# Kernel tuning notes

Hardware: AMD Instinct MI355X
Metric: run time of the kernel (lower is better)

Reference implementation:

```python
import jax, jax.numpy as jnp
import numpy as np

N_NODES = 50000
N_EDGES = 800000
IN_DIM = 128
HEADS = 8
HEAD_DIM = 16


def setup_inputs() -> dict:
    key = jax.random.key(0)
    ks = jax.random.split(key, 9)
    s = 1.0 / np.sqrt(IN_DIM)
    return {
        "h": jax.random.normal(ks[0], (N_NODES, IN_DIM), dtype=jnp.float32),
        "src": jax.random.randint(ks[1], (N_EDGES,), 0, N_NODES, dtype=jnp.int32),
        "dst": jax.random.randint(ks[2], (N_EDGES,), 0, N_NODES, dtype=jnp.int32),
        "WQ": jax.random.normal(ks[3], (IN_DIM, HEADS * HEAD_DIM), dtype=jnp.float32) * s,
        "bQ": jnp.zeros((HEADS * HEAD_DIM,), dtype=jnp.float32),
        "WK": jax.random.normal(ks[4], (IN_DIM, HEADS * HEAD_DIM), dtype=jnp.float32) * s,
        "bK": jnp.zeros((HEADS * HEAD_DIM,), dtype=jnp.float32),
        "WV": jax.random.normal(ks[5], (IN_DIM, HEADS * HEAD_DIM), dtype=jnp.float32) * s,
        "bV": jnp.zeros((HEADS * HEAD_DIM,), dtype=jnp.float32),
    }


def reference(h, src, dst, WQ, bQ, WK, bK, WV, bV):
    N = h.shape[0]
    sqrt_d = jnp.float32(np.sqrt(HEAD_DIM))
    # node projections, viewed as [N, H, D]
    Q = (h @ WQ + bQ).reshape(N, HEADS, HEAD_DIM)
    K = (h @ WK + bK).reshape(N, HEADS, HEAD_DIM)
    V = (h @ WV + bV).reshape(N, HEADS, HEAD_DIM)
    # edge scores: (K_src . Q_dst) per head, scaled exp with clamp [-5, 5]
    score = jnp.sum(K[src] * Q[dst], axis=-1, keepdims=True)  # [E, H, 1]
    score = jnp.exp(jnp.clip(score / sqrt_d, -5.0, 5.0))
    # segment-softmax denominator z and weighted V sum wV, both scattered to dst
    z = jax.ops.segment_sum(score, dst, num_segments=N)            # [N, H, 1]
    wV = jax.ops.segment_sum(V[src] * score, dst, num_segments=N)  # [N, H, D]
    # possible_empty: divide only where z > 0 (wV is 0 there anyway)
    head_out = jnp.where(z > 0, wV / jnp.where(z > 0, z, 1.0), wV)
    return head_out
```

## Files before the change

kernel.cpp:

```cpp
#include <hip/hip_runtime.h>
#include <math.h>

#define DIM 128
#define N_HEADS 8
#define HD 16
#define CAP 96

typedef __attribute__((ext_vector_type(8))) short bf16x8;
typedef __attribute__((ext_vector_type(4))) float f32x4;

__device__ __forceinline__ unsigned bf16pack2(float a, float b) {
    unsigned ua = __builtin_bit_cast(unsigned, a);
    unsigned ub = __builtin_bit_cast(unsigned, b);
    ua = (ua + 0x7FFFu + ((ua >> 16) & 1u)) >> 16;
    ub = (ub + 0x7FFFu + ((ub >> 16) & 1u)) >> 16;
    return ua | (ub << 16);
}
__device__ __forceinline__ float bf16lo(unsigned p) {
    return __builtin_bit_cast(float, p << 16);
}
__device__ __forceinline__ float bf16hi(unsigned p) {
    return __builtin_bit_cast(float, p & 0xFFFF0000u);
}

__global__ __launch_bounds__(256)
void init_kernel(const float* __restrict__ WQ, const float* __restrict__ bQ,
                 const float* __restrict__ WK, const float* __restrict__ bK,
                 const float* __restrict__ WV, const float* __restrict__ bV,
                 unsigned short* __restrict__ WT, float* __restrict__ bias384,
                 int* __restrict__ cnt, int NB, int N)
{
    if ((int)blockIdx.x < NB) {
        int i = blockIdx.x * 256 + threadIdx.x;
        if (i < N) cnt[i] = 0;
    } else {
        int idx = ((int)blockIdx.x - NB) * 256 + threadIdx.x;
        int c = idx >> 7, k = idx & 127;
        const float* W; const float* b; int col = c & 127;
        if (c < 128)      { W = WQ; b = bQ; }
        else if (c < 256) { W = WK; b = bK; }
        else              { W = WV; b = bV; }
        float v = W[k * DIM + col];
        WT[(size_t)c * DIM + k] = (unsigned short)(bf16pack2(v, 0.0f) & 0xFFFFu);
        if (k == 0) bias384[c] = b[col];
    }
}

__global__ __launch_bounds__(256)
void append_kernel(const int* __restrict__ src, const int* __restrict__ dst,
                   int* __restrict__ cnt, int* __restrict__ srcsF, int E)
{
    int e = blockIdx.x * 256 + threadIdx.x;
    if (e < E) {
        int d    = dst[e];
        int slot = atomicAdd(&cnt[d], 1);
        if (slot < CAP) srcsF[(size_t)d * CAP + slot] = src[e];
    }
}

__global__ __launch_bounds__(256)
void qkv_mfma_kernel(const float* __restrict__ h,
                     const unsigned short* __restrict__ WT,
                     const float* __restrict__ bias384,
                     unsigned* __restrict__ Qd, unsigned* __restrict__ KVd,
                     int N)
{
    __shared__ unsigned short hs[64 * 136];
    const int tid = threadIdx.x;
    const int n0  = blockIdx.x * 64;

    #pragma unroll
    for (int i = 0; i < 4; ++i) {
        int lin  = i * 256 + tid;
        int node = lin >> 4;
        int k0   = (lin & 15) * 8;
        int gn   = n0 + node;
        float4 a0, a1;
        if (gn < N) {
            a0 = *(const float4*)(h + (size_t)gn * DIM + k0);
            a1 = *(const float4*)(h + (size_t)gn * DIM + k0 + 4);
        } else {
            a0 = make_float4(0.f, 0.f, 0.f, 0.f);
            a1 = a0;
        }
        uint4 p = make_uint4(bf16pack2(a0.x, a0.y), bf16pack2(a0.z, a0.w),
                             bf16pack2(a1.x, a1.y), bf16pack2(a1.z, a1.w));
        *(uint4*)(hs + node * 136 + k0) = p;
    }
    __syncthreads();

    const int wave   = tid >> 6;
    const int l      = tid & 63;
    const int lane16 = l & 15;
    const int quad   = l >> 4;
    const int wc0    = wave * 96;

    f32x4 acc[6][4];
    #pragma unroll
    for (int ct = 0; ct < 6; ++ct) {
        float4 bv = *(const float4*)(bias384 + wc0 + ct * 16 + quad * 4);
        #pragma unroll
        for (int rt = 0; rt < 4; ++rt)
            acc[ct][rt] = (f32x4){bv.x, bv.y, bv.z, bv.w};
    }

    #pragma unroll
    for (int ks = 0; ks < 4; ++ks) {
        bf16x8 a[6], b[4];
        #pragma unroll
        for (int ct = 0; ct < 6; ++ct)
            a[ct] = *(const bf16x8*)(WT + (size_t)(wc0 + ct * 16 + lane16) * DIM
                                         + ks * 32 + quad * 8);
        #pragma unroll
        for (int rt = 0; rt < 4; ++rt)
            b[rt] = *(const bf16x8*)(hs + (rt * 16 + lane16) * 136 + ks * 32 + quad * 8);
        #pragma unroll
        for (int ct = 0; ct < 6; ++ct)
            #pragma unroll
            for (int rt = 0; rt < 4; ++rt)
                acc[ct][rt] = __builtin_amdgcn_mfma_f32_16x16x32_bf16(
                    a[ct], b[rt], acc[ct][rt], 0, 0, 0);
    }

    #pragma unroll
    for (int ct = 0; ct < 6; ++ct) {
        const int col = wc0 + ct * 16 + quad * 4;
        #pragma unroll
        for (int rt = 0; rt < 4; ++rt) {
            int gn = n0 + rt * 16 + lane16;
            if (gn >= N) continue;
            f32x4 v = acc[ct][rt];
            uint2 pr = make_uint2(bf16pack2(v[0], v[1]), bf16pack2(v[2], v[3]));
            if (col < 128) {
                *(uint2*)(Qd + (size_t)gn * 64 + (col >> 1)) = pr;
            } else if (col < 256) {
                int c = col - 128;
                *(uint2*)(KVd + (size_t)gn * 128 + ((c >> 3) * 8) + ((c & 4) >> 1)) = pr;
            } else {
                int c = col - 256;
                *(uint2*)(KVd + (size_t)gn * 128 + ((c >> 3) * 8) + 4 + ((c & 4) >> 1)) = pr;
            }
        }
    }
}

__global__ __launch_bounds__(256)
void aggregate_kernel(const int* __restrict__ cnt, const int* __restrict__ srcsF,
                      const unsigned* __restrict__ Qd, const unsigned* __restrict__ KVd,
                      float* __restrict__ out, int N)
{
    const int node = blockIdx.x * 4 + (threadIdx.x >> 6);
    if (node >= N) return;
    const int l    = threadIdx.x & 63;
    const int slot = l >> 4;
    const int c    = l & 15;

    const uint4 qd = *(const uint4*)(Qd + (size_t)node * 64 + c * 4);
    const float q0 = bf16lo(qd.x), q1 = bf16hi(qd.x);
    const float q2 = bf16lo(qd.y), q3 = bf16hi(qd.y);
    const float q4 = bf16lo(qd.z), q5 = bf16hi(qd.z);
    const float q6 = bf16lo(qd.w), q7 = bf16hi(qd.w);

    int deg = cnt[node];
    if (deg > CAP) deg = CAP;
    const int* bucket = srcsF + (size_t)node * CAP;

    float acc[8] = {0.f, 0.f, 0.f, 0.f, 0.f, 0.f, 0.f, 0.f};
    float zs = 0.f;

    for (int eg = 0; eg < deg; eg += 16) {
        bool val[4];
        const uint4* p[4];
        #pragma unroll
        for (int j = 0; j < 4; ++j) {
            int ee = eg + j * 4 + slot;
            val[j] = ee < deg;
            int s  = bucket[val[j] ? ee : (deg - 1)];
            p[j]   = (const uint4*)(KVd + (size_t)s * 128 + c * 8);
        }
        uint4 K[4], V[4];
        #pragma unroll
        for (int j = 0; j < 4; ++j) { K[j] = p[j][0]; V[j] = p[j][1]; }

        float d[4];
        #pragma unroll
        for (int j = 0; j < 4; ++j)
            d[j] = bf16lo(K[j].x) * q0 + bf16hi(K[j].x) * q1
                 + bf16lo(K[j].y) * q2 + bf16hi(K[j].y) * q3
                 + bf16lo(K[j].z) * q4 + bf16hi(K[j].z) * q5
                 + bf16lo(K[j].w) * q6 + bf16hi(K[j].w) * q7;
        #pragma unroll
        for (int j = 0; j < 4; ++j) d[j] += __shfl_xor(d[j], 1);

        #pragma unroll
        for (int j = 0; j < 4; ++j) {
            float pc = fminf(fmaxf(d[j] * 0.25f, -5.0f), 5.0f);
            float w  = val[j] ? __expf(pc) : 0.0f;
            zs += w;
            acc[0] += w * bf16lo(V[j].x); acc[1] += w * bf16hi(V[j].x);
            acc[2] += w * bf16lo(V[j].y); acc[3] += w * bf16hi(V[j].y);
            acc[4] += w * bf16lo(V[j].z); acc[5] += w * bf16hi(V[j].z);
            acc[6] += w * bf16lo(V[j].w); acc[7] += w * bf16hi(V[j].w);
        }
    }

    #pragma unroll
    for (int j = 0; j < 8; ++j) {
        acc[j] += __shfl_xor(acc[j], 16);
        acc[j] += __shfl_xor(acc[j], 32);
    }
    zs += __shfl_xor(zs, 16);
    zs += __shfl_xor(zs, 32);

    if (slot == 0) {
        float inv = (zs > 0.0f) ? (1.0f / zs) : 0.0f;
        *(float4*)(out + (size_t)node * DIM + c * 8) =
            make_float4(acc[0] * inv, acc[1] * inv, acc[2] * inv, acc[3] * inv);
        *(float4*)(out + (size_t)node * DIM + c * 8 + 4) =
            make_float4(acc[4] * inv, acc[5] * inv, acc[6] * inv, acc[7] * inv);
    }
}

extern "C" void kernel_launch(void* const* d_in, const int* in_sizes, int n_in,
                              void* d_out, int out_size, void* d_ws, size_t ws_size,
                              hipStream_t stream) {
    const float* h   = (const float*)d_in[0];
    const int*   src = (const int*)  d_in[1];
    const int*   dst = (const int*)  d_in[2];
    const float* WQ  = (const float*)d_in[3];
    const float* bQ  = (const float*)d_in[4];
    const float* WK  = (const float*)d_in[5];
    const float* bK  = (const float*)d_in[6];
    const float* WV  = (const float*)d_in[7];
    const float* bV  = (const float*)d_in[8];
    float* out = (float*)d_out;

    const int N  = in_sizes[0] / DIM;
    const int E  = in_sizes[1];
    const int NB = (N + 255) / 256;
    const int EB = (E + 255) / 256;
    const int nConv = (384 * DIM) / 256;

    char* w = (char*)d_ws;
    unsigned*       Qd      = (unsigned*)w;        w += (size_t)N * 64  * sizeof(unsigned);
    unsigned*       KVd     = (unsigned*)w;        w += (size_t)N * 128 * sizeof(unsigned);
    unsigned short* WT      = (unsigned short*)w;  w += (size_t)384 * DIM * sizeof(unsigned short);
    float*          bias384 = (float*)w;           w += 384 * sizeof(float);
    int*            cnt     = (int*)w;             w += (size_t)N * sizeof(int);
    int*            srcsF   = (int*)w;

    init_kernel<<<NB + nConv, 256, 0, stream>>>(WQ, bQ, WK, bK, WV, bV,
                                                WT, bias384, cnt, NB, N);
    append_kernel<<<EB, 256, 0, stream>>>(src, dst, cnt, srcsF, E);
    qkv_mfma_kernel<<<(N + 63) / 64, 256, 0, stream>>>(h, WT, bias384, Qd, KVd, N);
    aggregate_kernel<<<(N + 3) / 4, 256, 0, stream>>>(cnt, srcsF, Qd, KVd, out, N);
}
```

Before: 228.0 us.

## Merge edge bucketing with QKV projection and pipeline persistent aggregation

The edge-append work and the QKV MFMA projection now run in one launch, with the blocks split by index, so the scatter atomics overlap the GEMM and one launch is saved. The aggregate kernel becomes persistent: a fixed grid of 2048 blocks grid-strides over nodes and prefetches the next node's degree, Q and first 32 source indices while it processes the current one. The first two 16-edge chunks use these preloaded indices. This hides the dependent latency of loading an index and then gathering K/V, at the cost of more registers. The append blocks also allocate the 17KB shared array, which may lower their occupancy.

```diff
diff --git a/kernel.cpp b/kernel.cpp
--- a/kernel.cpp
+++ b/kernel.cpp
@@ -47,25 +47,26 @@
 }
 
 __global__ __launch_bounds__(256)
-void append_kernel(const int* __restrict__ src, const int* __restrict__ dst,
-                   int* __restrict__ cnt, int* __restrict__ srcsF, int E)
-{
-    int e = blockIdx.x * 256 + threadIdx.x;
-    if (e < E) {
-        int d    = dst[e];
-        int slot = atomicAdd(&cnt[d], 1);
-        if (slot < CAP) srcsF[(size_t)d * CAP + slot] = src[e];
-    }
-}
-
-__global__ __launch_bounds__(256)
-void qkv_mfma_kernel(const float* __restrict__ h,
-                     const unsigned short* __restrict__ WT,
-                     const float* __restrict__ bias384,
-                     unsigned* __restrict__ Qd, unsigned* __restrict__ KVd,
-                     int N)
+void append_qkv_kernel(const int* __restrict__ src, const int* __restrict__ dst,
+                       int* __restrict__ cnt, int* __restrict__ srcsF, int E, int QB,
+                       const float* __restrict__ h,
+                       const unsigned short* __restrict__ WT,
+                       const float* __restrict__ bias384,
+                       unsigned* __restrict__ Qd, unsigned* __restrict__ KVd,
+                       int N)
 {
     __shared__ unsigned short hs[64 * 136];
+
+    if ((int)blockIdx.x >= QB) {
+        int e = ((int)blockIdx.x - QB) * 256 + threadIdx.x;
+        if (e < E) {
+            int d    = dst[e];
+            int slot = atomicAdd(&cnt[d], 1);
+            if (slot < CAP) srcsF[(size_t)d * CAP + slot] = src[e];
+        }
+        return;
+    }
+
     const int tid = threadIdx.x;
     const int n0  = blockIdx.x * 64;
 
@@ -144,80 +145,134 @@
     }
 }
 
-__global__ __launch_bounds__(256)
+__device__ __forceinline__ void agg_chunk16(
+    const unsigned* __restrict__ KVd, int eg, int deg, int slot, int c,
+    const int* raw,
+    float q0, float q1, float q2, float q3,
+    float q4, float q5, float q6, float q7,
+    float acc[8], float& zs)
+{
+    bool val[4];
+    const uint4* p[4];
+    #pragma unroll
+    for (int j = 0; j < 4; ++j) {
+        int ee = eg + j * 4 + slot;
+        val[j] = ee < deg;
+        int s  = val[j] ? raw[j] : 0;
+        p[j]   = (const uint4*)(KVd + (size_t)s * 128 + c * 8);
+    }
+    uint4 K[4], V[4];
+    #pragma unroll
+    for (int j = 0; j < 4; ++j) { K[j] = p[j][0]; V[j] = p[j][1]; }
+
+    float d[4];
+    #pragma unroll
+    for (int j = 0; j < 4; ++j)
+        d[j] = bf16lo(K[j].x) * q0 + bf16hi(K[j].x) * q1
+             + bf16lo(K[j].y) * q2 + bf16hi(K[j].y) * q3
+             + bf16lo(K[j].z) * q4 + bf16hi(K[j].z) * q5
+             + bf16lo(K[j].w) * q6 + bf16hi(K[j].w) * q7;
+    #pragma unroll
+    for (int j = 0; j < 4; ++j) d[j] += __shfl_xor(d[j], 1);
+
+    #pragma unroll
+    for (int j = 0; j < 4; ++j) {
+        float pc = fminf(fmaxf(d[j] * 0.25f, -5.0f), 5.0f);
+        float w  = val[j] ? __expf(pc) : 0.0f;
+        zs += w;
+        acc[0] += w * bf16lo(V[j].x); acc[1] += w * bf16hi(V[j].x);
+        acc[2] += w * bf16lo(V[j].y); acc[3] += w * bf16hi(V[j].y);
+        acc[4] += w * bf16lo(V[j].z); acc[5] += w * bf16hi(V[j].z);
+        acc[6] += w * bf16lo(V[j].w); acc[7] += w * bf16hi(V[j].w);
+    }
+}
+
+__global__ __launch_bounds__(256, 4)
 void aggregate_kernel(const int* __restrict__ cnt, const int* __restrict__ srcsF,
                       const unsigned* __restrict__ Qd, const unsigned* __restrict__ KVd,
                       float* __restrict__ out, int N)
 {
-    const int node = blockIdx.x * 4 + (threadIdx.x >> 6);
+    const int l      = threadIdx.x & 63;
+    const int slot   = l >> 4;
+    const int c      = l & 15;
+    const int stride = gridDim.x * 4;
+
+    int node = blockIdx.x * 4 + (threadIdx.x >> 6);
     if (node >= N) return;
-    const int l    = threadIdx.x & 63;
-    const int slot = l >> 4;
-    const int c    = l & 15;
-
-    const uint4 qd = *(const uint4*)(Qd + (size_t)node * 64 + c * 4);
-    const float q0 = bf16lo(qd.x), q1 = bf16hi(qd.x);
-    const float q2 = bf16lo(qd.y), q3 = bf16hi(qd.y);
-    const float q4 = bf16lo(qd.z), q5 = bf16hi(qd.z);
-    const float q6 = bf16lo(qd.w), q7 = bf16hi(qd.w);
-
-    int deg = cnt[node];
-    if (deg > CAP) deg = CAP;
-    const int* bucket = srcsF + (size_t)node * CAP;
-
-    float acc[8] = {0.f, 0.f, 0.f, 0.f, 0.f, 0.f, 0.f, 0.f};
-    float zs = 0.f;
-
-    for (int eg = 0; eg < deg; eg += 16) {
-        bool val[4];
-        const uint4* p[4];
-        #pragma unroll
-        for (int j = 0; j < 4; ++j) {
-            int ee = eg + j * 4 + slot;
-            val[j] = ee < deg;
-            int s  = bucket[val[j] ? ee : (deg - 1)];
-            p[j]   = (const uint4*)(KVd + (size_t)s * 128 + c * 8);
-        }
-        uint4 K[4], V[4];
-        #pragma unroll
-        for (int j = 0; j < 4; ++j) { K[j] = p[j][0]; V[j] = p[j][1]; }
-
-        float d[4];
-        #pragma unroll
-        for (int j = 0; j < 4; ++j)
-            d[j] = bf16lo(K[j].x) * q0 + bf16hi(K[j].x) * q1
-                 + bf16lo(K[j].y) * q2 + bf16hi(K[j].y) * q3
-                 + bf16lo(K[j].z) * q4 + bf16hi(K[j].z) * q5
-                 + bf16lo(K[j].w) * q6 + bf16hi(K[j].w) * q7;
-        #pragma unroll
-        for (int j = 0; j < 4; ++j) d[j] += __shfl_xor(d[j], 1);
-
-        #pragma unroll
-        for (int j = 0; j < 4; ++j) {
-            float pc = fminf(fmaxf(d[j] * 0.25f, -5.0f), 5.0f);
-            float w  = val[j] ? __expf(pc) : 0.0f;
-            zs += w;
-            acc[0] += w * bf16lo(V[j].x); acc[1] += w * bf16hi(V[j].x);
-            acc[2] += w * bf16lo(V[j].y); acc[3] += w * bf16hi(V[j].y);
-            acc[4] += w * bf16lo(V[j].z); acc[5] += w * bf16hi(V[j].z);
-            acc[6] += w * bf16lo(V[j].w); acc[7] += w * bf16hi(V[j].w);
-        }
-    }
-
-    #pragma unroll
-    for (int j = 0; j < 8; ++j) {
-        acc[j] += __shfl_xor(acc[j], 16);
-        acc[j] += __shfl_xor(acc[j], 32);
-    }
-    zs += __shfl_xor(zs, 16);
-    zs += __shfl_xor(zs, 32);
-
-    if (slot == 0) {
-        float inv = (zs > 0.0f) ? (1.0f / zs) : 0.0f;
-        *(float4*)(out + (size_t)node * DIM + c * 8) =
-            make_float4(acc[0] * inv, acc[1] * inv, acc[2] * inv, acc[3] * inv);
-        *(float4*)(out + (size_t)node * DIM + c * 8 + 4) =
-            make_float4(acc[4] * inv, acc[5] * inv, acc[6] * inv, acc[7] * inv);
+
+    int   deg = cnt[node];
+    uint4 qd  = *(const uint4*)(Qd + (size_t)node * 64 + c * 4);
+    int   pb[8];
+    {
+        const int* b = srcsF + (size_t)node * CAP;
+        #pragma unroll
+        for (int j = 0; j < 8; ++j)
+            pb[j] = b[((j >> 2) << 4) + ((j & 3) << 2) + slot];
+    }
+
+    for (;;) {
+        const int  nnode   = node + stride;
+        const bool hasNext = nnode < N;
+
+        int ndeg = 0; uint4 nqd = make_uint4(0u, 0u, 0u, 0u); int npb[8];
+        #pragma unroll
+        for (int j = 0; j < 8; ++j) npb[j] = 0;
+        if (hasNext) {
+            ndeg = cnt[nnode];
+            nqd  = *(const uint4*)(Qd + (size_t)nnode * 64 + c * 4);
+            const int* b = srcsF + (size_t)nnode * CAP;
+            #pragma unroll
+            for (int j = 0; j < 8; ++j)
+                npb[j] = b[((j >> 2) << 4) + ((j & 3) << 2) + slot];
+        }
+
+        int degc = deg > CAP ? CAP : deg;
+        const float q0 = bf16lo(qd.x), q1 = bf16hi(qd.x);
+        const float q2 = bf16lo(qd.y), q3 = bf16hi(qd.y);
+        const float q4 = bf16lo(qd.z), q5 = bf16hi(qd.z);
+        const float q6 = bf16lo(qd.w), q7 = bf16hi(qd.w);
+
+        float acc[8] = {0.f, 0.f, 0.f, 0.f, 0.f, 0.f, 0.f, 0.f};
+        float zs = 0.f;
+
+        if (degc > 0)
+            agg_chunk16(KVd, 0, degc, slot, c, pb,
+                        q0, q1, q2, q3, q4, q5, q6, q7, acc, zs);
+        if (degc > 16)
+            agg_chunk16(KVd, 16, degc, slot, c, pb + 4,
+                        q0, q1, q2, q3, q4, q5, q6, q7, acc, zs);
+        for (int eg = 32; eg < degc; eg += 16) {
+            int raw[4];
+            const int* b = srcsF + (size_t)node * CAP;
+            #pragma unroll
+            for (int j = 0; j < 4; ++j) {
+                int ee = eg + j * 4 + slot;
+                raw[j] = b[ee < degc ? ee : 0];
+            }
+            agg_chunk16(KVd, eg, degc, slot, c, raw,
+                        q0, q1, q2, q3, q4, q5, q6, q7, acc, zs);
+        }
+
+        #pragma unroll
+        for (int j = 0; j < 8; ++j) {
+            acc[j] += __shfl_xor(acc[j], 16);
+            acc[j] += __shfl_xor(acc[j], 32);
+        }
+        zs += __shfl_xor(zs, 16);
+        zs += __shfl_xor(zs, 32);
+
+        if (slot == 0) {
+            float inv = (zs > 0.0f) ? (1.0f / zs) : 0.0f;
+            *(float4*)(out + (size_t)node * DIM + c * 8) =
+                make_float4(acc[0] * inv, acc[1] * inv, acc[2] * inv, acc[3] * inv);
+            *(float4*)(out + (size_t)node * DIM + c * 8 + 4) =
+                make_float4(acc[4] * inv, acc[5] * inv, acc[6] * inv, acc[7] * inv);
+        }
+
+        if (!hasNext) break;
+        node = nnode; deg = ndeg; qd = nqd;
+        #pragma unroll
+        for (int j = 0; j < 8; ++j) pb[j] = npb[j];
     }
 }
 
@@ -239,6 +294,7 @@
     const int E  = in_sizes[1];
     const int NB = (N + 255) / 256;
     const int EB = (E + 255) / 256;
+    const int QB = (N + 63) / 64;
     const int nConv = (384 * DIM) / 256;
 
     char* w = (char*)d_ws;
@@ -251,7 +307,7 @@
 
     init_kernel<<<NB + nConv, 256, 0, stream>>>(WQ, bQ, WK, bK, WV, bV,
                                                 WT, bias384, cnt, NB, N);
-    append_kernel<<<EB, 256, 0, stream>>>(src, dst, cnt, srcsF, E);
-    qkv_mfma_kernel<<<(N + 63) / 64, 256, 0, stream>>>(h, WT, bias384, Qd, KVd, N);
-    aggregate_kernel<<<(N + 3) / 4, 256, 0, stream>>>(cnt, srcsF, Qd, KVd, out, N);
-}
+    append_qkv_kernel<<<QB + EB, 256, 0, stream>>>(src, dst, cnt, srcsF, E, QB,
+                                                   h, WT, bias384, Qd, KVd, N);
+    aggregate_kernel<<<2048, 256, 0, stream>>>(cnt, srcsF, Qd, KVd, out, N);
+}
```

Result: faster. 223.4 us (-2.0%).
